# Kernel tuning notes

Measured on AMD Instinct MI355X. Metric: run time of the kernel, lower is better.

## Reference

```python
import jax, jax.numpy as jnp
import numpy as np

B, T, C = 4, 4096, 1024
NH, DH = 16, 128          # n_head, d_head = d_qkv // n_head
DQKV, DR = 2048, 256      # d_qkv, d_rank


def _uniform(key, shape, bound):
    return jax.random.uniform(key, shape, jnp.float32, -bound, bound)


def setup_inputs() -> dict:
    key = jax.random.key(0)
    k0, k1, k2, k3, k4 = jax.random.split(key, 5)
    # CastedLinear init: bound = sqrt(3) * 0.5 * in_features**-0.5 (same for w1, w2)
    b_qkv = (3 ** 0.5) * 0.5 * C ** (-0.5)
    b_proj = (3 ** 0.5) * 0.5 * DQKV ** (-0.5)
    return {
        "x": jax.random.normal(k0, (B, T, C), jnp.float32),
        "qkv_w1": _uniform(k1, (DR, C), b_qkv),
        "qkv_w2": _uniform(k2, (3 * DQKV, DR), b_qkv),
        "cproj_w1": _uniform(k3, (DR, DQKV), b_proj),
        "cproj_w2": _uniform(k4, (2 * C, DR), b_proj),
    }


def _rmsnorm(x):
    eps = jnp.finfo(x.dtype).eps  # F.rms_norm default eps
    return x * jax.lax.rsqrt(jnp.mean(x * x, axis=-1, keepdims=True) + eps)


def reference(x, qkv_w1, qkv_w2, cproj_w1, cproj_w2):
    Bx, Tx, Cx = x.shape
    # qkv projection with low-rank factorization + relu^2 activation between factors
    h = _rmsnorm(x) @ qkv_w1.T                      # [B,T,DR]
    h = jnp.square(jax.nn.relu(h))
    qkv = (h @ qkv_w2.T).reshape(Bx, Tx, 3 * NH, DH)
    q, k, v = jnp.split(qkv, 3, axis=2)             # each [B,T,NH,DH]
    q, k = _rmsnorm(q), _rmsnorm(k)

    # rotary embedding: half the head dim rotated, second quarter frequencies zero
    quarter = DH // 4
    freq = (1.0 / 1024.0) ** jnp.linspace(0.0, 1.0, quarter)
    freq = jnp.concatenate([freq, jnp.zeros(quarter, freq.dtype)])  # [DH//2]
    theta = jnp.arange(Tx, dtype=jnp.float32)[:, None] * freq[None, :]
    cos = jnp.cos(theta)[None, :, None, :]          # [1,T,1,DH//2]
    sin = jnp.sin(theta)[None, :, None, :]

    def rope(z):
        z1, z2 = jnp.split(z, 2, axis=-1)
        return jnp.concatenate([z1 * cos + z2 * sin, -z1 * sin + z2 * cos], axis=-1)

    q, k = rope(q), rope(k)

    # causal linear attention: sigmoid-gated cumulative sum over time
    y = jax.nn.relu(q) * jnp.cumsum(jax.nn.sigmoid(k) * v, axis=1)  # [B,T,NH,DH]
    y = y.reshape(Bx, Tx, NH * DH)

    # low-rank output projection (no activation), gated residual
    uv = (y @ cproj_w1.T) @ cproj_w2.T              # [B,T,2C]
    u, g = jnp.split(uv, 2, axis=-1)
    return x + u * jax.nn.silu(g)
```

## Files before the change

kernel.cpp:

```cpp
#include <hip/hip_runtime.h>
#include <hip/hip_bf16.h>

#define TB 4
#define TT 4096
#define TC 1024
#define TNH 16
#define TDH 128
#define TDQKV 2048
#define TDR 256
#define RB 4096
#define ROWS (TB*TT)

typedef __attribute__((ext_vector_type(8))) short bfx8;
typedef __attribute__((ext_vector_type(4))) float fx4;
typedef __attribute__((address_space(1))) const unsigned char GAS;
typedef __attribute__((address_space(3))) unsigned char LAS;

__device__ __forceinline__ unsigned short f2b(float f) {
    unsigned int u = __float_as_uint(f);
    unsigned int r = (u + 0x7fffu + ((u >> 16) & 1u)) >> 16;
    return (unsigned short)r;
}
__device__ __forceinline__ float b2f(unsigned short h) {
    return __uint_as_float(((unsigned int)h) << 16);
}
__device__ __forceinline__ float sigm(float x) {
    return 1.0f / (1.0f + __expf(-x));
}
__device__ __forceinline__ int xcd_swz(int hw, int nwg) {
    int q = nwg >> 3;
    return (hw & 7) * q + (hw >> 3);
}

__global__ __launch_bounds__(256) void setup_all(const float* __restrict__ wq1, unsigned short* __restrict__ w1b,
                                                 const float* __restrict__ wq2, unsigned short* __restrict__ w2b,
                                                 const float* __restrict__ wc1, unsigned short* __restrict__ wp1b,
                                                 const float* __restrict__ wc2, unsigned short* __restrict__ wp2b,
                                                 float* __restrict__ ct, float* __restrict__ st) {
    int blk = blockIdx.x;
    if (blk < 2816) {
        const float* in; unsigned short* out; int base;
        if (blk < 256)       { in = wq1; out = w1b;  base = blk; }
        else if (blk < 1792) { in = wq2; out = w2b;  base = blk - 256; }
        else if (blk < 2304) { in = wc1; out = wp1b; base = blk - 1792; }
        else                 { in = wc2; out = wp2b; base = blk - 2304; }
        int i = (base * 256 + threadIdx.x) * 4;
        float4 v = *(const float4*)(in + i);
        out[i + 0] = f2b(v.x);
        out[i + 1] = f2b(v.y);
        out[i + 2] = f2b(v.z);
        out[i + 3] = f2b(v.w);
    } else {
        int i = (blk - 2816) * 256 + threadIdx.x;
        int t = i >> 5, j = i & 31;
        float fr = exp2f(-10.0f * (float)j / 31.0f);
        float th = (float)t * fr;
        ct[i] = cosf(th);
        st[i] = sinf(th);
    }
}

__global__ __launch_bounds__(256) void rmsnorm_x(const float* __restrict__ x,
                                                 unsigned short* __restrict__ xn) {
    int row = blockIdx.x;
    int tid = threadIdx.x;
    float4 v = *(const float4*)(x + (size_t)row * TC + tid * 4);
    float ss = v.x * v.x + v.y * v.y + v.z * v.z + v.w * v.w;
    #pragma unroll
    for (int o = 32; o > 0; o >>= 1) ss += __shfl_xor(ss, o);
    __shared__ float red[4];
    if ((tid & 63) == 0) red[tid >> 6] = ss;
    __syncthreads();
    float tot = red[0] + red[1] + red[2] + red[3];
    float sc = rsqrtf(tot * (1.0f / TC) + 1.1920929e-7f);
    unsigned short* o = xn + (size_t)row * TC + tid * 4;
    o[0] = f2b(v.x * sc); o[1] = f2b(v.y * sc); o[2] = f2b(v.z * sc); o[3] = f2b(v.w * sc);
}

__global__ __launch_bounds__(256) void gemm2v(const unsigned short* __restrict__ A, int lda,
                                              const unsigned short* __restrict__ Bm,
                                              unsigned short* __restrict__ C,
                                              int K, size_t slab) {
    __shared__ unsigned short As[2][128 * 32];
    __shared__ unsigned short Bs[2][128 * 32];
    const int m0 = blockIdx.y * 128;
    const int n0 = blockIdx.x * 128;
    const int tid = threadIdx.x;
    const int lane = tid & 63;
    const int w = tid >> 6;
    const int wr = w >> 1, wc = w & 1;
    const int r16 = lane & 15;
    const int rg = lane >> 4;
    const int kk = rg * 8;
    const int l4 = lane >> 2;
    const int c8 = (lane & 3) * 8;
    const int nk = K >> 5;
    fx4 acc[4][4] = {};

    auto stage = [&](int buf, int k0) {
        #pragma unroll
        for (int i = 0; i < 2; ++i) {
            int rr = (w + 4 * i) * 16 + l4;
            const unsigned short* ga = A + (size_t)(m0 + rr) * lda + k0 + c8;
            const unsigned short* gb = Bm + (size_t)(n0 + rr) * K + k0 + c8;
            __builtin_amdgcn_global_load_lds((GAS*)ga, (LAS*)&As[buf][(w + 4 * i) * 512], 16, 0, 0);
            __builtin_amdgcn_global_load_lds((GAS*)gb, (LAS*)&Bs[buf][(w + 4 * i) * 512], 16, 0, 0);
        }
    };

    stage(0, 0);
    __syncthreads();
    int buf = 0;
    for (int ks = 0; ks < nk; ++ks) {
        if (ks + 1 < nk) stage(buf ^ 1, (ks + 1) * 32);
        bfx8 af[4], bfr[4];
        #pragma unroll
        for (int mi = 0; mi < 4; mi++) af[mi] = *(const bfx8*)&As[buf][(wr * 64 + mi * 16 + r16) * 32 + kk];
        #pragma unroll
        for (int ni = 0; ni < 4; ni++) bfr[ni] = *(const bfx8*)&Bs[buf][(wc * 64 + ni * 16 + r16) * 32 + kk];
        #pragma unroll
        for (int mi = 0; mi < 4; mi++)
            #pragma unroll
            for (int ni = 0; ni < 4; ni++)
                acc[mi][ni] = __builtin_amdgcn_mfma_f32_16x16x32_bf16(bfr[ni], af[mi], acc[mi][ni], 0, 0, 0);
        __syncthreads();
        buf ^= 1;
    }

    unsigned short* dst = C + (size_t)(n0 >> 7) * slab;
    #pragma unroll
    for (int mi = 0; mi < 4; mi++) {
        int m = m0 + wr * 64 + mi * 16 + r16;
        #pragma unroll
        for (int ni = 0; ni < 4; ni++) {
            int nloc = wc * 64 + ni * 16 + rg * 4;
            ushort4 o;
            o.x = f2b(acc[mi][ni][0]); o.y = f2b(acc[mi][ni][1]);
            o.z = f2b(acc[mi][ni][2]); o.w = f2b(acc[mi][ni][3]);
            *(ushort4*)(dst + (size_t)m * 128 + nloc) = o;
        }
    }
}

template <int EPI, int NX>
__global__ __launch_bounds__(256) void gemm_sk(const unsigned short* __restrict__ A, int lda,
                                               const unsigned short* __restrict__ Bm,
                                               unsigned short* __restrict__ C, int ldc,
                                               int K) {
    __shared__ unsigned short As[2][128 * 32];
    __shared__ unsigned short Bs[2][64 * 32];
    const int lg = xcd_swz(blockIdx.x, gridDim.x);
    const int n0 = (lg % NX) * 64;
    const int m0 = (lg / NX) * 128;
    const int tid = threadIdx.x;
    const int lane = tid & 63;
    const int w = tid >> 6;
    const int wr = w >> 1, wc = w & 1;
    const int r16 = lane & 15;
    const int rg = lane >> 4;
    const int kk = rg * 8;
    const int l4 = lane >> 2;
    const int c8 = (lane & 3) * 8;
    const int nk = K >> 5;
    fx4 acc[4][2] = {};

    auto stage = [&](int buf, int k0) {
        #pragma unroll
        for (int i = 0; i < 2; ++i) {
            int rr = (w + 4 * i) * 16 + l4;
            const unsigned short* ga = A + (size_t)(m0 + rr) * lda + k0 + c8;
            __builtin_amdgcn_global_load_lds((GAS*)ga, (LAS*)&As[buf][(w + 4 * i) * 512], 16, 0, 0);
        }
        const unsigned short* gb = Bm + (size_t)(n0 + w * 16 + l4) * K + k0 + c8;
        __builtin_amdgcn_global_load_lds((GAS*)gb, (LAS*)&Bs[buf][w * 512], 16, 0, 0);
    };

    stage(0, 0);
    __syncthreads();
    int buf = 0;
    for (int ks = 0; ks < nk; ++ks) {
        if (ks + 1 < nk) stage(buf ^ 1, (ks + 1) * 32);
        bfx8 af[4], bfr[2];
        #pragma unroll
        for (int mi = 0; mi < 4; mi++) af[mi] = *(const bfx8*)&As[buf][(wr * 64 + mi * 16 + r16) * 32 + kk];
        #pragma unroll
        for (int ni = 0; ni < 2; ni++) bfr[ni] = *(const bfx8*)&Bs[buf][(wc * 32 + ni * 16 + r16) * 32 + kk];
        #pragma unroll
        for (int mi = 0; mi < 4; mi++)
            #pragma unroll
            for (int ni = 0; ni < 2; ni++)
                acc[mi][ni] = __builtin_amdgcn_mfma_f32_16x16x32_bf16(bfr[ni], af[mi], acc[mi][ni], 0, 0, 0);
        __syncthreads();
        buf ^= 1;
    }

    #pragma unroll
    for (int mi = 0; mi < 4; mi++) {
        int m = m0 + wr * 64 + mi * 16 + r16;
        #pragma unroll
        for (int ni = 0; ni < 2; ni++) {
            int n = n0 + wc * 32 + ni * 16 + rg * 4;
            ushort4 o;
            #pragma unroll
            for (int j = 0; j < 4; ++j) {
                float v = acc[mi][ni][j];
                if (EPI == 1) { v = fmaxf(v, 0.0f); v *= v; }
                ((unsigned short*)&o)[j] = f2b(v);
            }
            *(ushort4*)(C + (size_t)m * ldc + n) = o;
        }
    }
}

__global__ __launch_bounds__(256) void gemm4f64(const unsigned short* __restrict__ A,
                                                const unsigned short* __restrict__ Wm,
                                                const float* __restrict__ x,
                                                float* __restrict__ out) {
    __shared__ unsigned short As[2][64 * 32];
    __shared__ unsigned short Bu[2][64 * 32];
    __shared__ unsigned short Bg[2][64 * 32];
    const int hw = blockIdx.y * gridDim.x + blockIdx.x;
    const int lg = xcd_swz(hw, gridDim.x * gridDim.y);
    const int n0 = (lg & 15) * 64;
    const int m0 = (lg >> 4) * 64;
    const int tid = threadIdx.x;
    const int lane = tid & 63;
    const int w = tid >> 6;
    const int wr = w >> 1, wc = w & 1;
    const int r16 = lane & 15;
    const int rg = lane >> 4;
    const int kk = rg * 8;
    const int l4 = lane >> 2;
    const int c8 = (lane & 3) * 8;
    fx4 accu[2][2] = {};
    fx4 accg[2][2] = {};

    auto stage = [&](int buf, int k0) {
        int rr = w * 16 + l4;
        const unsigned short* ga = A + (size_t)(m0 + rr) * TDR + k0 + c8;
        const unsigned short* gu = Wm + (size_t)(n0 + rr) * TDR + k0 + c8;
        const unsigned short* gg = Wm + (size_t)(1024 + n0 + rr) * TDR + k0 + c8;
        __builtin_amdgcn_global_load_lds((GAS*)ga, (LAS*)&As[buf][w * 512], 16, 0, 0);
        __builtin_amdgcn_global_load_lds((GAS*)gu, (LAS*)&Bu[buf][w * 512], 16, 0, 0);
        __builtin_amdgcn_global_load_lds((GAS*)gg, (LAS*)&Bg[buf][w * 512], 16, 0, 0);
    };

    stage(0, 0);
    __syncthreads();
    int buf = 0;
    for (int ks = 0; ks < 8; ++ks) {
        if (ks + 1 < 8) stage(buf ^ 1, (ks + 1) * 32);
        bfx8 af[2], bu[2], bg[2];
        #pragma unroll
        for (int mi = 0; mi < 2; mi++) af[mi] = *(const bfx8*)&As[buf][(wr * 32 + mi * 16 + r16) * 32 + kk];
        #pragma unroll
        for (int ni = 0; ni < 2; ni++) {
            bu[ni] = *(const bfx8*)&Bu[buf][(wc * 32 + ni * 16 + r16) * 32 + kk];
            bg[ni] = *(const bfx8*)&Bg[buf][(wc * 32 + ni * 16 + r16) * 32 + kk];
        }
        #pragma unroll
        for (int mi = 0; mi < 2; mi++)
            #pragma unroll
            for (int ni = 0; ni < 2; ni++) {
                accu[mi][ni] = __builtin_amdgcn_mfma_f32_16x16x32_bf16(bu[ni], af[mi], accu[mi][ni], 0, 0, 0);
                accg[mi][ni] = __builtin_amdgcn_mfma_f32_16x16x32_bf16(bg[ni], af[mi], accg[mi][ni], 0, 0, 0);
            }
        __syncthreads();
        buf ^= 1;
    }

    #pragma unroll
    for (int mi = 0; mi < 2; mi++) {
        int m = m0 + wr * 32 + mi * 16 + r16;
        #pragma unroll
        for (int ni = 0; ni < 2; ni++) {
            int n = n0 + wc * 32 + ni * 16 + rg * 4;
            size_t base = (size_t)m * TC + n;
            float4 xv = *(const float4*)(x + base);
            float4 o;
            #pragma unroll
            for (int j = 0; j < 4; ++j) {
                float u = accu[mi][ni][j];
                float g = accg[mi][ni][j];
                (&o.x)[j] = (&xv.x)[j] + u * (g * sigm(g));
            }
            *(float4*)(out + base) = o;
        }
    }
}

__global__ __launch_bounds__(256) void post64(unsigned short* __restrict__ qkv,
                                              const float* __restrict__ ct,
                                              const float* __restrict__ st,
                                              float* __restrict__ part,
                                              int ntiles, int nseg) {
    const int blk = blockIdx.x;
    const int tile = blk % ntiles, h = blk / ntiles;
    const size_t slab = (size_t)ntiles * 64 * 128;
    const int g = threadIdx.x >> 4, l16 = threadIdx.x & 15;
    const int d0 = l16 * 4;
    unsigned short* qs = qkv + (size_t)h * slab;
    unsigned short* ks = qkv + (size_t)(16 + h) * slab;
    unsigned short* vs = qkv + (size_t)(32 + h) * slab;
    __shared__ float psum[2][16][128];
    float acc0[2][4] = {};
    float acc1[2][4] = {};

    #pragma unroll
    for (int p = 0; p < 4; ++p) {
        const int r = tile * 64 + p * 16 + g;
        const int t = r & (TT - 1);
        const size_t lo = (size_t)r * 128 + d0, hi = lo + 64;
        ushort4 q1 = *(const ushort4*)(qs + lo);
        ushort4 q2 = *(const ushort4*)(qs + hi);
        ushort4 k1 = *(const ushort4*)(ks + lo);
        ushort4 k2 = *(const ushort4*)(ks + hi);
        float qa[8] = {b2f(q1.x), b2f(q1.y), b2f(q1.z), b2f(q1.w),
                       b2f(q2.x), b2f(q2.y), b2f(q2.z), b2f(q2.w)};
        float ka[8] = {b2f(k1.x), b2f(k1.y), b2f(k1.z), b2f(k1.w),
                       b2f(k2.x), b2f(k2.y), b2f(k2.z), b2f(k2.w)};
        float ssq = 0.0f, ssk = 0.0f;
        #pragma unroll
        for (int j = 0; j < 8; ++j) { ssq += qa[j] * qa[j]; ssk += ka[j] * ka[j]; }
        #pragma unroll
        for (int o = 8; o > 0; o >>= 1) {
            ssq += __shfl_xor(ssq, o);
            ssk += __shfl_xor(ssk, o);
        }
        float qsc = rsqrtf(ssq * (1.0f / TDH) + 1.1920929e-7f);
        float ksc = rsqrtf(ssk * (1.0f / TDH) + 1.1920929e-7f);
        float c[4], s[4];
        if (l16 < 8) {
            float4 cv = *(const float4*)(ct + t * 32 + d0);
            float4 sv = *(const float4*)(st + t * 32 + d0);
            c[0] = cv.x; c[1] = cv.y; c[2] = cv.z; c[3] = cv.w;
            s[0] = sv.x; s[1] = sv.y; s[2] = sv.z; s[3] = sv.w;
        } else {
            c[0] = c[1] = c[2] = c[3] = 1.0f;
            s[0] = s[1] = s[2] = s[3] = 0.0f;
        }
        ushort4 v1 = *(const ushort4*)(vs + lo);
        ushort4 v2 = *(const ushort4*)(vs + hi);
        float va[8] = {b2f(v1.x), b2f(v1.y), b2f(v1.z), b2f(v1.w),
                       b2f(v2.x), b2f(v2.y), b2f(v2.z), b2f(v2.w)};
        ushort4 qo1, qo2, po1, po2;
        unsigned short* qo1p = (unsigned short*)&qo1;
        unsigned short* qo2p = (unsigned short*)&qo2;
        unsigned short* po1p = (unsigned short*)&po1;
        unsigned short* po2p = (unsigned short*)&po2;
        const int h2 = p >> 1;
        #pragma unroll
        for (int j = 0; j < 4; ++j) {
            float z1q = qa[j] * qsc, z2q = qa[4 + j] * qsc;
            float z1k = ka[j] * ksc, z2k = ka[4 + j] * ksc;
            float qlo = z1q * c[j] + z2q * s[j];
            float qhi = z2q * c[j] - z1q * s[j];
            float klo = z1k * c[j] + z2k * s[j];
            float khi = z2k * c[j] - z1k * s[j];
            float plo = sigm(klo) * va[j];
            float phi = sigm(khi) * va[4 + j];
            qo1p[j] = f2b(qlo); qo2p[j] = f2b(qhi);
            po1p[j] = f2b(plo); po2p[j] = f2b(phi);
            acc0[h2][j] += plo;
            acc1[h2][j] += phi;
        }
        *(ushort4*)(qs + lo) = qo1;
        *(ushort4*)(qs + hi) = qo2;
        *(ushort4*)(ks + lo) = po1;
        *(ushort4*)(ks + hi) = po2;
    }
    #pragma unroll
    for (int h2 = 0; h2 < 2; ++h2) {
        *(float4*)&psum[h2][g][d0]      = *(float4*)acc0[h2];
        *(float4*)&psum[h2][g][64 + d0] = *(float4*)acc1[h2];
    }
    __syncthreads();
    const int h2 = threadIdx.x >> 7, d = threadIdx.x & 127;
    float tot = 0.0f;
    #pragma unroll
    for (int gg = 0; gg < 16; ++gg) tot += psum[h2][gg][d];
    part[((size_t)h * nseg + tile * 2 + h2) * 128 + d] = tot;
}

__global__ __launch_bounds__(256) void scanB2(float* __restrict__ part, int cb) {
    int idx = blockIdx.x * 256 + threadIdx.x;
    int d = idx & 127;
    int hb = idx >> 7;
    int batch = hb % cb;
    int h = hb / cb;
    int nseg = cb * 128;
    size_t base = ((size_t)h * nseg + (size_t)batch * 128) * 128 + d;
    float run = 0.0f;
    #pragma unroll
    for (int r = 0; r < 4; ++r) {
        float v[32];
        #pragma unroll
        for (int i = 0; i < 32; ++i) v[i] = part[base + (size_t)(r * 32 + i) * 128];
        #pragma unroll
        for (int i = 0; i < 32; ++i) { float tv = v[i]; v[i] = run; run += tv; }
        #pragma unroll
        for (int i = 0; i < 32; ++i) part[base + (size_t)(r * 32 + i) * 128] = v[i];
    }
}

__global__ __launch_bounds__(256) void scanC3(const unsigned short* __restrict__ qkv,
                                              const float* __restrict__ part,
                                              unsigned short* __restrict__ y,
                                              int nsegblk, int nseg) {
    const int bseg = blockIdx.x % nsegblk, h = blockIdx.x / nsegblk;
    const size_t slab = (size_t)nseg * 32 * 128;
    const int g = threadIdx.x >> 4, l16 = threadIdx.x & 15;
    const int seg = bseg * 16 + g;
    const int d0 = l16 * 8;
    const unsigned short* qp = qkv + (size_t)h * slab;
    const unsigned short* pp = qkv + (size_t)(16 + h) * slab;
    float sum[8];
    const float* pb = part + ((size_t)h * nseg + seg) * 128 + d0;
    *(float4*)&sum[0] = *(const float4*)pb;
    *(float4*)&sum[4] = *(const float4*)(pb + 4);
    #pragma unroll 4
    for (int i = 0; i < 32; ++i) {
        int t = seg * 32 + i;
        size_t off = (size_t)t * 128 + d0;
        bfx8 pv = *(const bfx8*)(pp + off);
        bfx8 qv = *(const bfx8*)(qp + off);
        bfx8 ov;
        #pragma unroll
        for (int j = 0; j < 8; ++j) {
            sum[j] += b2f((unsigned short)pv[j]);
            float q = b2f((unsigned short)qv[j]);
            ov[j] = (short)f2b(fmaxf(q, 0.0f) * sum[j]);
        }
        *(bfx8*)(y + (size_t)t * 2048 + h * 128 + d0) = ov;
    }
}

extern "C" void kernel_launch(void* const* d_in, const int* in_sizes, int n_in,
                              void* d_out, int out_size, void* d_ws, size_t ws_size,
                              hipStream_t stream) {
    (void)in_sizes; (void)n_in; (void)out_size;
    const float* x    = (const float*)d_in[0];
    const float* wq1  = (const float*)d_in[1];
    const float* wq2  = (const float*)d_in[2];
    const float* wc1  = (const float*)d_in[3];
    const float* wc2  = (const float*)d_in[4];
    float* out = (float*)d_out;

    auto need = [](int cb) -> size_t {
        size_t o = 0;
        auto a = [&](size_t b) { o = (o + 255) & ~(size_t)255; o += b; };
        size_t qkvsz = (size_t)cb * RB * 6144 * 2;
        size_t xnsz  = (size_t)ROWS * TC * 2;
        a(qkvsz > xnsz ? qkvsz : xnsz);
        a((size_t)ROWS * TDR * 2);
        a((size_t)TDR * TC * 2);
        a((size_t)3 * TDQKV * TDR * 2);
        a((size_t)TDR * TDQKV * 2);
        a((size_t)2 * TC * TDR * 2);
        a((size_t)TT * 32 * 4);
        a((size_t)TT * 32 * 4);
        a((size_t)TNH * (cb * RB / 32) * 128 * 4);
        return o;
    };
    int CB = (ws_size >= need(4)) ? 4 : (ws_size >= need(2)) ? 2 : 1;
    const int TR = CB * RB;
    const int NCH = TB / CB;
    const int nseg = TR / 32;
    const int ntiles = TR / 64;

    char* ws = (char*)d_ws;
    size_t off = 0;
    auto alloc = [&](size_t bytes) -> void* {
        off = (off + 255) & ~(size_t)255;
        void* p = ws + off;
        off += bytes;
        return p;
    };
    size_t qkvsz = (size_t)TR * 6144 * 2;
    size_t xnsz  = (size_t)ROWS * TC * 2;
    char* pool = (char*)alloc(qkvsz > xnsz ? qkvsz : xnsz);
    unsigned short* qkvb = (unsigned short*)pool;
    unsigned short* xn   = (unsigned short*)pool;
    unsigned short* t1   = (unsigned short*)pool;
    unsigned short* hbuf = (unsigned short*)alloc((size_t)ROWS * TDR * 2);
    unsigned short* w1b  = (unsigned short*)alloc((size_t)TDR * TC * 2);
    unsigned short* w2b  = (unsigned short*)alloc((size_t)3 * TDQKV * TDR * 2);
    unsigned short* wp1b = (unsigned short*)alloc((size_t)TDR * TDQKV * 2);
    unsigned short* wp2b = (unsigned short*)alloc((size_t)2 * TC * TDR * 2);
    float* ct   = (float*)alloc((size_t)TT * 32 * 4);
    float* st   = (float*)alloc((size_t)TT * 32 * 4);
    float* part = (float*)alloc((size_t)TNH * nseg * 128 * 4);
    unsigned short* ybuf = (unsigned short*)d_out;

    setup_all<<<3328, 256, 0, stream>>>(wq1, w1b, wq2, w2b, wc1, wp1b, wc2, wp2b, ct, st);

    rmsnorm_x<<<ROWS, 256, 0, stream>>>(x, xn);
    gemm_sk<1, 4><<<(ROWS / 128) * (TDR / 64), 256, 0, stream>>>(
        xn, TC, w1b, hbuf, TDR, TC);

    for (int c = 0; c < NCH; ++c) {
        gemm2v<<<dim3(6144 / 128, TR / 128), 256, 0, stream>>>(
            hbuf + (size_t)c * TR * TDR, TDR, w2b, qkvb, TDR, (size_t)TR * 128);
        post64<<<TNH * ntiles, 256, 0, stream>>>(qkvb, ct, st, part, ntiles, nseg);
        scanB2<<<(TNH * CB * 128) / 256, 256, 0, stream>>>(part, CB);
        scanC3<<<TNH * (nseg / 16), 256, 0, stream>>>(
            qkvb, part, ybuf + (size_t)c * TR * 2048, nseg / 16, nseg);
    }

    gemm_sk<0, 4><<<(ROWS / 128) * (TDR / 64), 256, 0, stream>>>(
        ybuf, 2048, wp1b, t1, TDR, TDQKV);
    gemm4f64<<<dim3(TC / 64, ROWS / 64), 256, 0, stream>>>(t1, wp2b, x, out);
}
```

Baseline: 364.4 us.

## Recompute q/k norm and rope in scan kernels instead of writing back

Removes the post64 pass that normalized and rotated q/k, wrote back q and sigmoid(k)*v into the qkv buffer, and produced segment partial sums. A new sumKV kernel reads k and v to produce the partials, and scanCY recomputes the norm, rope and gating for q, k and v inline while emitting y. This avoids writing q and the k*v product back to memory, at the cost of reading k twice and doing the transcendental work twice. The GEMM epilogue also switches from vector ushort4 stores to scalar per-element stores with swapped MFMA operands, which may hurt store coalescing.

```diff
diff --git a/kernel.cpp b/kernel.cpp
--- a/kernel.cpp
+++ b/kernel.cpp
@@ -77,10 +77,11 @@
     o[0] = f2b(v.x * sc); o[1] = f2b(v.y * sc); o[2] = f2b(v.z * sc); o[3] = f2b(v.w * sc);
 }
 
-__global__ __launch_bounds__(256) void gemm2v(const unsigned short* __restrict__ A, int lda,
-                                              const unsigned short* __restrict__ Bm,
-                                              unsigned short* __restrict__ C,
-                                              int K, size_t slab) {
+template <int EPI>
+__global__ __launch_bounds__(256) void gemm_bt(const unsigned short* __restrict__ A, int lda,
+                                               const unsigned short* __restrict__ Bm,
+                                               unsigned short* __restrict__ C, int ldc,
+                                               int N, int K, size_t slab) {
     __shared__ unsigned short As[2][128 * 32];
     __shared__ unsigned short Bs[2][128 * 32];
     const int m0 = blockIdx.y * 128;
@@ -90,8 +91,7 @@
     const int w = tid >> 6;
     const int wr = w >> 1, wc = w & 1;
     const int r16 = lane & 15;
-    const int rg = lane >> 4;
-    const int kk = rg * 8;
+    const int kk = (lane >> 4) * 8;
     const int l4 = lane >> 2;
     const int c8 = (lane & 3) * 8;
     const int nk = K >> 5;
@@ -122,24 +122,30 @@
         for (int mi = 0; mi < 4; mi++)
             #pragma unroll
             for (int ni = 0; ni < 4; ni++)
-                acc[mi][ni] = __builtin_amdgcn_mfma_f32_16x16x32_bf16(bfr[ni], af[mi], acc[mi][ni], 0, 0, 0);
+                acc[mi][ni] = __builtin_amdgcn_mfma_f32_16x16x32_bf16(af[mi], bfr[ni], acc[mi][ni], 0, 0, 0);
         __syncthreads();
         buf ^= 1;
     }
 
-    unsigned short* dst = C + (size_t)(n0 >> 7) * slab;
+    const int rg = lane >> 4;
     #pragma unroll
-    for (int mi = 0; mi < 4; mi++) {
-        int m = m0 + wr * 64 + mi * 16 + r16;
+    for (int mi = 0; mi < 4; mi++)
         #pragma unroll
         for (int ni = 0; ni < 4; ni++) {
-            int nloc = wc * 64 + ni * 16 + rg * 4;
-            ushort4 o;
-            o.x = f2b(acc[mi][ni][0]); o.y = f2b(acc[mi][ni][1]);
-            o.z = f2b(acc[mi][ni][2]); o.w = f2b(acc[mi][ni][3]);
-            *(ushort4*)(dst + (size_t)m * 128 + nloc) = o;
-        }
-    }
+            int col = n0 + wc * 64 + ni * 16 + r16;
+            #pragma unroll
+            for (int r = 0; r < 4; r++) {
+                int row = m0 + wr * 64 + mi * 16 + rg * 4 + r;
+                float v = acc[mi][ni][r];
+                if (EPI == 1) { v = fmaxf(v, 0.0f); v *= v; }
+                if (EPI == 2) {
+                    int head = col >> 7;
+                    C[(size_t)head * slab + (size_t)row * 128 + (col & 127)] = f2b(v);
+                } else {
+                    C[(size_t)row * ldc + col] = f2b(v);
+                }
+            }
+        }
 }
 
 template <int EPI, int NX>
@@ -289,97 +295,62 @@
     }
 }
 
-__global__ __launch_bounds__(256) void post64(unsigned short* __restrict__ qkv,
-                                              const float* __restrict__ ct,
-                                              const float* __restrict__ st,
-                                              float* __restrict__ part,
-                                              int ntiles, int nseg) {
-    const int blk = blockIdx.x;
-    const int tile = blk % ntiles, h = blk / ntiles;
-    const size_t slab = (size_t)ntiles * 64 * 128;
+__global__ __launch_bounds__(256) void sumKV(const unsigned short* __restrict__ qkv,
+                                             const float* __restrict__ ct,
+                                             const float* __restrict__ st,
+                                             float* __restrict__ part,
+                                             int nsegblk, int nseg) {
+    const int bseg = blockIdx.x % nsegblk, h = blockIdx.x / nsegblk;
+    const size_t slab = (size_t)nseg * 32 * 128;
     const int g = threadIdx.x >> 4, l16 = threadIdx.x & 15;
-    const int d0 = l16 * 4;
-    unsigned short* qs = qkv + (size_t)h * slab;
-    unsigned short* ks = qkv + (size_t)(16 + h) * slab;
-    unsigned short* vs = qkv + (size_t)(32 + h) * slab;
-    __shared__ float psum[2][16][128];
-    float acc0[2][4] = {};
-    float acc1[2][4] = {};
-
-    #pragma unroll
-    for (int p = 0; p < 4; ++p) {
-        const int r = tile * 64 + p * 16 + g;
-        const int t = r & (TT - 1);
-        const size_t lo = (size_t)r * 128 + d0, hi = lo + 64;
-        ushort4 q1 = *(const ushort4*)(qs + lo);
-        ushort4 q2 = *(const ushort4*)(qs + hi);
-        ushort4 k1 = *(const ushort4*)(ks + lo);
-        ushort4 k2 = *(const ushort4*)(ks + hi);
-        float qa[8] = {b2f(q1.x), b2f(q1.y), b2f(q1.z), b2f(q1.w),
-                       b2f(q2.x), b2f(q2.y), b2f(q2.z), b2f(q2.w)};
-        float ka[8] = {b2f(k1.x), b2f(k1.y), b2f(k1.z), b2f(k1.w),
-                       b2f(k2.x), b2f(k2.y), b2f(k2.z), b2f(k2.w)};
-        float ssq = 0.0f, ssk = 0.0f;
-        #pragma unroll
-        for (int j = 0; j < 8; ++j) { ssq += qa[j] * qa[j]; ssk += ka[j] * ka[j]; }
-        #pragma unroll
-        for (int o = 8; o > 0; o >>= 1) {
-            ssq += __shfl_xor(ssq, o);
-            ssk += __shfl_xor(ssk, o);
-        }
-        float qsc = rsqrtf(ssq * (1.0f / TDH) + 1.1920929e-7f);
+    const int seg = bseg * 16 + g;
+    const int d0 = l16 * 8;
+    const int dl = (l16 & 7) * 8;
+    const bool rot = dl < 32;
+    const float se = (l16 < 8) ? 1.0f : -1.0f;
+    const unsigned short* kp = qkv + (size_t)(16 + h) * slab;
+    const unsigned short* vp = qkv + (size_t)(32 + h) * slab;
+    float sum[8] = {};
+    #pragma unroll 2
+    for (int i = 0; i < 32; ++i) {
+        const int t = seg * 32 + i;
+        const int tt = t & (TT - 1);
+        const size_t off = (size_t)t * 128 + d0;
+        bfx8 k8 = *(const bfx8*)(kp + off);
+        bfx8 v8 = *(const bfx8*)(vp + off);
+        float ka[8];
+        float ssk = 0.0f;
+        #pragma unroll
+        for (int j = 0; j < 8; ++j) { ka[j] = b2f((unsigned short)k8[j]); ssk += ka[j] * ka[j]; }
+        #pragma unroll
+        for (int o = 1; o < 16; o <<= 1) ssk += __shfl_xor(ssk, o);
         float ksc = rsqrtf(ssk * (1.0f / TDH) + 1.1920929e-7f);
-        float c[4], s[4];
-        if (l16 < 8) {
-            float4 cv = *(const float4*)(ct + t * 32 + d0);
-            float4 sv = *(const float4*)(st + t * 32 + d0);
-            c[0] = cv.x; c[1] = cv.y; c[2] = cv.z; c[3] = cv.w;
-            s[0] = sv.x; s[1] = sv.y; s[2] = sv.z; s[3] = sv.w;
+        #pragma unroll
+        for (int j = 0; j < 8; ++j) ka[j] *= ksc;
+        float kb[8];
+        #pragma unroll
+        for (int j = 0; j < 8; ++j) kb[j] = __shfl_xor(ka[j], 8);
+        float c[8], s[8];
+        if (rot) {
+            float4 c0 = *(const float4*)(ct + tt * 32 + dl);
+            float4 c1 = *(const float4*)(ct + tt * 32 + dl + 4);
+            float4 s0 = *(const float4*)(st + tt * 32 + dl);
+            float4 s1 = *(const float4*)(st + tt * 32 + dl + 4);
+            c[0]=c0.x; c[1]=c0.y; c[2]=c0.z; c[3]=c0.w; c[4]=c1.x; c[5]=c1.y; c[6]=c1.z; c[7]=c1.w;
+            s[0]=s0.x; s[1]=s0.y; s[2]=s0.z; s[3]=s0.w; s[4]=s1.x; s[5]=s1.y; s[6]=s1.z; s[7]=s1.w;
         } else {
-            c[0] = c[1] = c[2] = c[3] = 1.0f;
-            s[0] = s[1] = s[2] = s[3] = 0.0f;
-        }
-        ushort4 v1 = *(const ushort4*)(vs + lo);
-        ushort4 v2 = *(const ushort4*)(vs + hi);
-        float va[8] = {b2f(v1.x), b2f(v1.y), b2f(v1.z), b2f(v1.w),
-                       b2f(v2.x), b2f(v2.y), b2f(v2.z), b2f(v2.w)};
-        ushort4 qo1, qo2, po1, po2;
-        unsigned short* qo1p = (unsigned short*)&qo1;
-        unsigned short* qo2p = (unsigned short*)&qo2;
-        unsigned short* po1p = (unsigned short*)&po1;
-        unsigned short* po2p = (unsigned short*)&po2;
-        const int h2 = p >> 1;
-        #pragma unroll
-        for (int j = 0; j < 4; ++j) {
-            float z1q = qa[j] * qsc, z2q = qa[4 + j] * qsc;
-            float z1k = ka[j] * ksc, z2k = ka[4 + j] * ksc;
-            float qlo = z1q * c[j] + z2q * s[j];
-            float qhi = z2q * c[j] - z1q * s[j];
-            float klo = z1k * c[j] + z2k * s[j];
-            float khi = z2k * c[j] - z1k * s[j];
-            float plo = sigm(klo) * va[j];
-            float phi = sigm(khi) * va[4 + j];
-            qo1p[j] = f2b(qlo); qo2p[j] = f2b(qhi);
-            po1p[j] = f2b(plo); po2p[j] = f2b(phi);
-            acc0[h2][j] += plo;
-            acc1[h2][j] += phi;
-        }
-        *(ushort4*)(qs + lo) = qo1;
-        *(ushort4*)(qs + hi) = qo2;
-        *(ushort4*)(ks + lo) = po1;
-        *(ushort4*)(ks + hi) = po2;
-    }
-    #pragma unroll
-    for (int h2 = 0; h2 < 2; ++h2) {
-        *(float4*)&psum[h2][g][d0]      = *(float4*)acc0[h2];
-        *(float4*)&psum[h2][g][64 + d0] = *(float4*)acc1[h2];
-    }
-    __syncthreads();
-    const int h2 = threadIdx.x >> 7, d = threadIdx.x & 127;
-    float tot = 0.0f;
-    #pragma unroll
-    for (int gg = 0; gg < 16; ++gg) tot += psum[h2][gg][d];
-    part[((size_t)h * nseg + tile * 2 + h2) * 128 + d] = tot;
+            #pragma unroll
+            for (int j = 0; j < 8; ++j) { c[j] = 1.0f; s[j] = 0.0f; }
+        }
+        #pragma unroll
+        for (int j = 0; j < 8; ++j) {
+            float kr = ka[j] * c[j] + kb[j] * (s[j] * se);
+            sum[j] += sigm(kr) * b2f((unsigned short)v8[j]);
+        }
+    }
+    float* pb = part + ((size_t)h * nseg + seg) * 128 + d0;
+    *(float4*)pb = *(float4*)&sum[0];
+    *(float4*)(pb + 4) = *(float4*)&sum[4];
 }
 
 __global__ __launch_bounds__(256) void scanB2(float* __restrict__ part, int cb) {
@@ -403,33 +374,70 @@
     }
 }
 
-__global__ __launch_bounds__(256) void scanC3(const unsigned short* __restrict__ qkv,
+__global__ __launch_bounds__(256) void scanCY(const unsigned short* __restrict__ qkv,
                                               const float* __restrict__ part,
                                               unsigned short* __restrict__ y,
+                                              const float* __restrict__ ct,
+                                              const float* __restrict__ st,
                                               int nsegblk, int nseg) {
     const int bseg = blockIdx.x % nsegblk, h = blockIdx.x / nsegblk;
     const size_t slab = (size_t)nseg * 32 * 128;
     const int g = threadIdx.x >> 4, l16 = threadIdx.x & 15;
     const int seg = bseg * 16 + g;
     const int d0 = l16 * 8;
+    const int dl = (l16 & 7) * 8;
+    const bool rot = dl < 32;
+    const float se = (l16 < 8) ? 1.0f : -1.0f;
     const unsigned short* qp = qkv + (size_t)h * slab;
-    const unsigned short* pp = qkv + (size_t)(16 + h) * slab;
+    const unsigned short* kp = qkv + (size_t)(16 + h) * slab;
+    const unsigned short* vp = qkv + (size_t)(32 + h) * slab;
     float sum[8];
     const float* pb = part + ((size_t)h * nseg + seg) * 128 + d0;
     *(float4*)&sum[0] = *(const float4*)pb;
     *(float4*)&sum[4] = *(const float4*)(pb + 4);
-    #pragma unroll 4
+    #pragma unroll 2
     for (int i = 0; i < 32; ++i) {
-        int t = seg * 32 + i;
-        size_t off = (size_t)t * 128 + d0;
-        bfx8 pv = *(const bfx8*)(pp + off);
-        bfx8 qv = *(const bfx8*)(qp + off);
+        const int t = seg * 32 + i;
+        const int tt = t & (TT - 1);
+        const size_t off = (size_t)t * 128 + d0;
+        bfx8 q8 = *(const bfx8*)(qp + off);
+        bfx8 k8 = *(const bfx8*)(kp + off);
+        bfx8 v8 = *(const bfx8*)(vp + off);
+        float qa[8], ka[8];
+        float ssq = 0.0f, ssk = 0.0f;
+        #pragma unroll
+        for (int j = 0; j < 8; ++j) {
+            qa[j] = b2f((unsigned short)q8[j]); ssq += qa[j] * qa[j];
+            ka[j] = b2f((unsigned short)k8[j]); ssk += ka[j] * ka[j];
+        }
+        #pragma unroll
+        for (int o = 1; o < 16; o <<= 1) { ssq += __shfl_xor(ssq, o); ssk += __shfl_xor(ssk, o); }
+        float qsc = rsqrtf(ssq * (1.0f / TDH) + 1.1920929e-7f);
+        float ksc = rsqrtf(ssk * (1.0f / TDH) + 1.1920929e-7f);
+        #pragma unroll
+        for (int j = 0; j < 8; ++j) { qa[j] *= qsc; ka[j] *= ksc; }
+        float qb[8], kb[8];
+        #pragma unroll
+        for (int j = 0; j < 8; ++j) { qb[j] = __shfl_xor(qa[j], 8); kb[j] = __shfl_xor(ka[j], 8); }
+        float c[8], s[8];
+        if (rot) {
+            float4 c0 = *(const float4*)(ct + tt * 32 + dl);
+            float4 c1 = *(const float4*)(ct + tt * 32 + dl + 4);
+            float4 s0 = *(const float4*)(st + tt * 32 + dl);
+            float4 s1 = *(const float4*)(st + tt * 32 + dl + 4);
+            c[0]=c0.x; c[1]=c0.y; c[2]=c0.z; c[3]=c0.w; c[4]=c1.x; c[5]=c1.y; c[6]=c1.z; c[7]=c1.w;
+            s[0]=s0.x; s[1]=s0.y; s[2]=s0.z; s[3]=s0.w; s[4]=s1.x; s[5]=s1.y; s[6]=s1.z; s[7]=s1.w;
+        } else {
+            #pragma unroll
+            for (int j = 0; j < 8; ++j) { c[j] = 1.0f; s[j] = 0.0f; }
+        }
         bfx8 ov;
         #pragma unroll
         for (int j = 0; j < 8; ++j) {
-            sum[j] += b2f((unsigned short)pv[j]);
-            float q = b2f((unsigned short)qv[j]);
-            ov[j] = (short)f2b(fmaxf(q, 0.0f) * sum[j]);
+            float qr = qa[j] * c[j] + qb[j] * (s[j] * se);
+            float kr = ka[j] * c[j] + kb[j] * (s[j] * se);
+            sum[j] += sigm(kr) * b2f((unsigned short)v8[j]);
+            ov[j] = (short)f2b(fmaxf(qr, 0.0f) * sum[j]);
         }
         *(bfx8*)(y + (size_t)t * 2048 + h * 128 + d0) = ov;
     }
@@ -467,6 +475,7 @@
     const int NCH = TB / CB;
     const int nseg = TR / 32;
     const int ntiles = TR / 64;
+    (void)ntiles;
 
     char* ws = (char*)d_ws;
     size_t off = 0;
@@ -499,12 +508,12 @@
         xn, TC, w1b, hbuf, TDR, TC);
 
     for (int c = 0; c < NCH; ++c) {
-        gemm2v<<<dim3(6144 / 128, TR / 128), 256, 0, stream>>>(
-            hbuf + (size_t)c * TR * TDR, TDR, w2b, qkvb, TDR, (size_t)TR * 128);
-        post64<<<TNH * ntiles, 256, 0, stream>>>(qkvb, ct, st, part, ntiles, nseg);
+        gemm_bt<2><<<dim3(6144 / 128, TR / 128), 256, 0, stream>>>(
+            hbuf + (size_t)c * TR * TDR, TDR, w2b, qkvb, 0, 6144, TDR, (size_t)TR * 128);
+        sumKV<<<TNH * (nseg / 16), 256, 0, stream>>>(qkvb, ct, st, part, nseg / 16, nseg);
         scanB2<<<(TNH * CB * 128) / 256, 256, 0, stream>>>(part, CB);
-        scanC3<<<TNH * (nseg / 16), 256, 0, stream>>>(
-            qkvb, part, ybuf + (size_t)c * TR * 2048, nseg / 16, nseg);
+        scanCY<<<TNH * (nseg / 16), 256, 0, stream>>>(
+            qkvb, part, ybuf + (size_t)c * TR * 2048, ct, st, nseg / 16, nseg);
     }
 
     gemm_sk<0, 4><<<(ROWS / 128) * (TDR / 64), 256, 0, stream>>>(
```

Result: no change. 366.7 us (+0.6%).
